# Kernel optimization log

Measured on AMD Instinct MI355X. Metric: run time of the kernel, lower is better.

The kernel has to match this reference:

```python
import jax, jax.numpy as jnp
import numpy as np

FILTER_SIZE = 3  # from init_kwargs


def setup_inputs() -> dict:
    key = jax.random.key(0)
    k1, k2 = jax.random.split(key)
    B, C, H, W = 4, 3, 384, 1248
    left_input = jax.random.uniform(k1, (B, C, H, W), dtype=jnp.float32)
    right_input = jax.random.uniform(k2, (B, C, H, W), dtype=jnp.float32)
    return {"left_input": left_input, "right_input": right_input}


def _extract_patches(x, f):
    # Faithful to conv3d with one-hot (identity) filters of kernel (1,f,f),
    # padding (0, f//2, f//2): out[b, k*C+c, y, x] = x_padded[b, c, y+dy, x+dx]
    B, C, H, W = x.shape
    pad = f // 2
    xp = jnp.pad(x, ((0, 0), (0, 0), (pad, pad), (pad, pad)))
    # [B, f*f, C, H, W]: shift index k = dy*f + dx (row-major over kernel window)
    patches = jnp.stack(
        [xp[:, :, dy:dy + H, dx:dx + W] for dy in range(f) for dx in range(f)],
        axis=1,
    )
    return patches.reshape(B, f * f * C, H, W)


def reference(left_input, right_input):
    f = FILTER_SIZE
    left_features = _extract_patches(left_input, f)
    right_features = _extract_patches(right_input, f)
    # one_hot_filter[k, 0, 0, i, j] = 1 iff i*f + j == k (identity unfold filter)
    one_hot_filter = jnp.eye(f * f, dtype=jnp.float32).reshape(f * f, 1, 1, f, f)
    return (left_features, right_features, one_hot_filter)
```

## Files before the change

kernel.cpp:

```cpp
#include <hip/hip_runtime.h>

#define B_ 4
#define C_ 3
#define H_ 384
#define W_ 1248
#define F_ 3
#define KK_ 9
#define W4_ (W_ / 4)

constexpr int N_FEAT = B_ * KK_ * C_ * H_ * W_;
constexpr int N4     = N_FEAT / 4;

__global__ __launch_bounds__(256) void unfold_kernel(
    const float* __restrict__ left,
    const float* __restrict__ right,
    float* __restrict__ out)
{
    int idx = blockIdx.x * blockDim.x + threadIdx.x;
    const int total = 2 * N4;
    if (idx >= total) return;

    const float* in = left;
    float* o = out;
    int t = idx;
    if (t >= N4) { t -= N4; in = right; o = out + N_FEAT; }

    int x4 = t % W4_;
    int r  = t / W4_;
    int y  = r % H_;
    int r2 = r / H_;
    int c  = r2 % C_;
    int r3 = r2 / C_;
    int k  = r3 % KK_;
    int b  = r3 / KK_;

    int dy = k / F_ - 1;
    int dx = k % F_ - 1;
    int yin = y + dy;

    float4 v = make_float4(0.f, 0.f, 0.f, 0.f);
    if (yin >= 0 && yin < H_) {
        const float* row = in + ((size_t)((b * C_ + c) * H_ + yin)) * W_;
        int x0 = x4 * 4;
        if (dx == 0) {
            v = *reinterpret_cast<const float4*>(row + x0);
        } else {
            float tmp[4];
            #pragma unroll
            for (int j = 0; j < 4; ++j) {
                int xin = x0 + j + dx;
                tmp[j] = (xin >= 0 && xin < W_) ? row[xin] : 0.f;
            }
            v = make_float4(tmp[0], tmp[1], tmp[2], tmp[3]);
        }
    }
    *reinterpret_cast<float4*>(o + (size_t)t * 4) = v;
}

__global__ void onehot_kernel(float* __restrict__ out)
{
    int i = threadIdx.x;
    if (i < KK_ * KK_) out[i] = (i % 10 == 0) ? 1.0f : 0.0f;
}

extern "C" void kernel_launch(void* const* d_in, const int* in_sizes, int n_in,
                              void* d_out, int out_size, void* d_ws, size_t ws_size,
                              hipStream_t stream)
{
    const float* left  = (const float*)d_in[0];
    const float* right = (const float*)d_in[1];
    float* out = (float*)d_out;

    const int total4 = 2 * N4;
    int blocks = (total4 + 255) / 256;
    unfold_kernel<<<blocks, 256, 0, stream>>>(left, right, out);
    onehot_kernel<<<1, 128, 0, stream>>>(out + (size_t)2 * N_FEAT);
}
```

Measured before the change: 458.6 us.

## Compute all nine shifted patches per thread from shared row loads

Each thread now loads three input rows (a float4 plus left and right neighbours) for both left and right inputs, then writes all nine shifted output planes. This replaces one-thread-per-output-float4, which redid index decoding and scalar unaligned loads for every shift. It reduces redundant loads and integer math, at the cost of 18x fewer threads with many more stores each, which could affect latency hiding.

```diff
diff --git a/kernel.cpp b/kernel.cpp
--- a/kernel.cpp
+++ b/kernel.cpp
@@ -9,52 +9,64 @@
 #define W4_ (W_ / 4)
 
 constexpr int N_FEAT = B_ * KK_ * C_ * H_ * W_;
-constexpr int N4     = N_FEAT / 4;
+constexpr int NTH    = B_ * C_ * H_ * W4_;
 
-__global__ __launch_bounds__(256) void unfold_kernel(
+__global__ __launch_bounds__(256) void unfold9_kernel(
     const float* __restrict__ left,
     const float* __restrict__ right,
     float* __restrict__ out)
 {
-    int idx = blockIdx.x * blockDim.x + threadIdx.x;
-    const int total = 2 * N4;
-    if (idx >= total) return;
-
-    const float* in = left;
-    float* o = out;
-    int t = idx;
-    if (t >= N4) { t -= N4; in = right; o = out + N_FEAT; }
+    int t = blockIdx.x * blockDim.x + threadIdx.x;
+    if (t >= NTH) return;
 
     int x4 = t % W4_;
     int r  = t / W4_;
     int y  = r % H_;
     int r2 = r / H_;
     int c  = r2 % C_;
-    int r3 = r2 / C_;
-    int k  = r3 % KK_;
-    int b  = r3 / KK_;
+    int b  = r2 / C_;
+    int x0 = x4 * 4;
 
-    int dy = k / F_ - 1;
-    int dx = k % F_ - 1;
-    int yin = y + dy;
+    const size_t inbase = ((size_t)(b * C_ + c)) * H_ * W_;
+    const float* ins[2] = { left, right };
 
-    float4 v = make_float4(0.f, 0.f, 0.f, 0.f);
-    if (yin >= 0 && yin < H_) {
-        const float* row = in + ((size_t)((b * C_ + c) * H_ + yin)) * W_;
-        int x0 = x4 * 4;
-        if (dx == 0) {
-            v = *reinterpret_cast<const float4*>(row + x0);
-        } else {
-            float tmp[4];
-            #pragma unroll
-            for (int j = 0; j < 4; ++j) {
-                int xin = x0 + j + dx;
-                tmp[j] = (xin >= 0 && xin < W_) ? row[xin] : 0.f;
+    float4 m[2][3];
+    float  lf[2][3], rg[2][3];
+
+    #pragma unroll
+    for (int s = 0; s < 2; ++s) {
+        #pragma unroll
+        for (int dy = 0; dy < 3; ++dy) {
+            int yin = y + dy - 1;
+            if (yin >= 0 && yin < H_) {
+                const float* rp = ins[s] + inbase + (size_t)yin * W_;
+                m[s][dy]  = *reinterpret_cast<const float4*>(rp + x0);
+                lf[s][dy] = (x0 > 0)        ? rp[x0 - 1] : 0.f;
+                rg[s][dy] = (x0 + 4 < W_)   ? rp[x0 + 4] : 0.f;
+            } else {
+                m[s][dy]  = make_float4(0.f, 0.f, 0.f, 0.f);
+                lf[s][dy] = 0.f;
+                rg[s][dy] = 0.f;
             }
-            v = make_float4(tmp[0], tmp[1], tmp[2], tmp[3]);
         }
     }
-    *reinterpret_cast<float4*>(o + (size_t)t * 4) = v;
+
+    const size_t row_off = (((size_t)(b * KK_) * C_ + c) * H_ + y) * W_ + x0;
+    const size_t kstride = (size_t)C_ * H_ * W_;
+
+    #pragma unroll
+    for (int s = 0; s < 2; ++s) {
+        float* ob = out + (size_t)s * N_FEAT + row_off;
+        #pragma unroll
+        for (int dy = 0; dy < 3; ++dy) {
+            float4 mm = m[s][dy];
+            float4 vL = make_float4(lf[s][dy], mm.x, mm.y, mm.z);
+            float4 vR = make_float4(mm.y, mm.z, mm.w, rg[s][dy]);
+            *reinterpret_cast<float4*>(ob + (size_t)(dy * 3 + 0) * kstride) = vL;
+            *reinterpret_cast<float4*>(ob + (size_t)(dy * 3 + 1) * kstride) = mm;
+            *reinterpret_cast<float4*>(ob + (size_t)(dy * 3 + 2) * kstride) = vR;
+        }
+    }
 }
 
 __global__ void onehot_kernel(float* __restrict__ out)
@@ -71,8 +83,7 @@
     const float* right = (const float*)d_in[1];
     float* out = (float*)d_out;
 
-    const int total4 = 2 * N4;
-    int blocks = (total4 + 255) / 256;
-    unfold_kernel<<<blocks, 256, 0, stream>>>(left, right, out);
+    int blocks = (NTH + 255) / 256;
+    unfold9_kernel<<<blocks, 256, 0, stream>>>(left, right, out);
     onehot_kernel<<<1, 128, 0, stream>>>(out + (size_t)2 * N_FEAT);
 }
```

New measurement: 443.7 us. 3.3% less time.
